# Kernel optimization log

Measured on AMD Instinct MI355X. Metric: run time of the kernel, lower is better.

## Reference

```python
import jax, jax.numpy as jnp
import numpy as np

MODES = 8
WIDTH = 20
LAYERS = 4
TI = 20
B, SX, SY, T = 4, 128, 128, 20


def setup_inputs() -> dict:
    key = jax.random.key(0)
    ks = jax.random.split(key, 12)
    scale = 1.0 / (WIDTH * WIDTH)
    x = jax.random.normal(ks[0], (B, SX, SY, T), jnp.float32)
    # spectral weights: 4 corner blocks per layer, complex stored as real/imag
    spec_wr = scale * jax.random.uniform(ks[1], (LAYERS, 4, WIDTH, WIDTH, MODES, MODES, MODES), jnp.float32)
    spec_wi = scale * jax.random.uniform(ks[2], (LAYERS, 4, WIDTH, WIDTH, MODES, MODES, MODES), jnp.float32)
    conv_w = 0.1 * jax.random.normal(ks[3], (LAYERS, WIDTH, WIDTH), jnp.float32)  # 1x1 conv over channels
    conv_b = 0.01 * jax.random.normal(ks[4], (LAYERS, WIDTH), jnp.float32)
    fc0_w = 0.05 * jax.random.normal(ks[5], (TI + 3, WIDTH), jnp.float32)
    fc0_b = jnp.zeros((WIDTH,), jnp.float32)
    fc1_w = 0.05 * jax.random.normal(ks[6], (WIDTH, 128), jnp.float32)
    fc1_b = jnp.zeros((128,), jnp.float32)
    fc2_w = 0.05 * jax.random.normal(ks[7], (128, 1), jnp.float32)
    fc2_b = jnp.zeros((1,), jnp.float32)
    return {"x": x, "spec_wr": spec_wr, "spec_wi": spec_wi, "conv_w": conv_w,
            "conv_b": conv_b, "fc0_w": fc0_w, "fc0_b": fc0_b, "fc1_w": fc1_w,
            "fc1_b": fc1_b, "fc2_w": fc2_w, "fc2_b": fc2_b}


def _spectral_conv(h, w):
    # h: [B, C, X, Y, Z] real; w: [4, C, C, m, m, m] complex
    b, c, X, Y, Z = h.shape
    m = MODES
    hft = jnp.fft.rfftn(h, axes=(-3, -2, -1))  # [B,C,X,Y,Z//2+1]
    mul = lambda a, wt: jnp.einsum('bixyz,ioxyz->boxyz', a, wt)
    out = jnp.zeros((b, c, X, Y, Z // 2 + 1), jnp.complex64)
    out = out.at[:, :, :m, :m, :m].set(mul(hft[:, :, :m, :m, :m], w[0]))
    out = out.at[:, :, -m:, :m, :m].set(mul(hft[:, :, -m:, :m, :m], w[1]))
    out = out.at[:, :, :m, -m:, :m].set(mul(hft[:, :, :m, -m:, :m], w[2]))
    out = out.at[:, :, -m:, -m:, :m].set(mul(hft[:, :, -m:, -m:, :m], w[3]))
    return jnp.fft.irfftn(out, s=(X, Y, Z), axes=(-3, -2, -1))


def reference(x, spec_wr, spec_wi, conv_w, conv_b, fc0_w, fc0_b, fc1_w, fc1_b, fc2_w, fc2_b):
    b, sx, sy, st = x.shape
    f32 = x.dtype
    # grids in [0,1]; gridt = linspace(0,1,T+1)[1:]
    gx = jnp.linspace(0.0, 1.0, sx, dtype=f32)[None, :, None, None, None]
    gy = jnp.linspace(0.0, 1.0, sy, dtype=f32)[None, None, :, None, None]
    gt = jnp.linspace(0.0, 1.0, st + 1, dtype=f32)[1:][None, None, None, :, None]
    shp = (b, sx, sy, st, 1)
    xr = jnp.broadcast_to(x[:, :, :, None, :], (b, sx, sy, st, st))  # repeat over new T axis
    feat = jnp.concatenate([jnp.broadcast_to(gx, shp), jnp.broadcast_to(gy, shp),
                            jnp.broadcast_to(gt, shp), xr], axis=-1)  # [B,Sx,Sy,T,T+3]
    h = feat @ fc0_w + fc0_b                       # [B,Sx,Sy,T,W]
    h = jnp.transpose(h, (0, 4, 1, 2, 3))          # [B,W,Sx,Sy,T]
    for l in range(LAYERS):
        w = (spec_wr[l] + 1j * spec_wi[l]).astype(jnp.complex64)
        sup = _spectral_conv(h, w)
        inf = jnp.einsum('bixyz,oi->boxyz', h, conv_w[l]) + conv_b[l][None, :, None, None, None]
        h = jax.nn.relu(sup + inf)
    h = jnp.transpose(h, (0, 2, 3, 4, 1))          # [B,Sx,Sy,T,W]
    h = jax.nn.relu(h @ fc1_w + fc1_b)
    out = h @ fc2_w + fc2_b                        # [B,Sx,Sy,T,1]
    return out
```

## Files before the change

kernel.cpp:

```cpp
#include <hip/hip_runtime.h>


#define BB 4
#define CC 20
#define NX 128
#define NY 128
#define NZ 20
#define MM 8
#define NKX 16
#define NKY 16
#define NKZ 8
#define CH_STRIDE (NX * NY * NZ)

#define OFF_H    0u
#define OFF_T1   26214400u
#define OFF_T2   32768000u
#define OFF_A    33587200u
#define OFF_AOUT 33914880u
#define OFF_WXY  34242560u
#define OFF_WZ   34246656u

__global__ void k_tables(float* __restrict__ Wxy, float* __restrict__ Wz) {
    int tid = blockIdx.x * blockDim.x + threadIdx.x;
    const double PI2 = 6.283185307179586476925286766559;
    if (tid < NX * NKX) {
        int y = tid >> 4, ki = tid & 15;
        int kphys = (ki < MM) ? ki : (NX - NKX + ki);
        int p = (y * kphys) & (NX - 1);
        double ang = -PI2 * (double)p / (double)NX;
        Wxy[2 * tid]     = (float)cos(ang);
        Wxy[2 * tid + 1] = (float)sin(ang);
    } else if (tid < NX * NKX + NZ * NKZ) {
        int t = tid - NX * NKX;
        int z = t >> 3, kz = t & 7;
        int p = (z * kz) % NZ;
        double ang = -PI2 * (double)p / (double)NZ;
        Wz[2 * t]     = (float)cos(ang);
        Wz[2 * t + 1] = (float)sin(ang);
    }
}

__global__ __launch_bounds__(256) void k_fc0(const float* __restrict__ x,
                                             const float* __restrict__ w0,
                                             const float* __restrict__ b0,
                                             float* __restrict__ h) {
    int tid = blockIdx.x * blockDim.x + threadIdx.x;
    if (tid >= BB * CC * NX * NY) return;
    int y = tid & 127;
    int r = tid >> 7;
    int xx = r & 127; r >>= 7;
    int c = r % CC;
    int b = r / CC;
    const float* xp = x + (((size_t)(b * NX + xx)) * NY + y) * NZ;
    float base = b0[c] + ((float)xx / 127.0f) * w0[0 * CC + c]
                       + ((float)y  / 127.0f) * w0[1 * CC + c];
#pragma unroll
    for (int k = 0; k < 20; k++) base = fmaf(xp[k], w0[(3 + k) * CC + c], base);
    float wt = w0[2 * CC + c];
    float* hp = h + (size_t)tid * NZ;
#pragma unroll
    for (int t = 0; t < 20; t++) hp[t] = base + ((float)(t + 1) / 20.0f) * wt;
}

__global__ __launch_bounds__(320) void k_dft_y(const float* __restrict__ h,
                                               const float* __restrict__ Wxy,
                                               float* __restrict__ t1) {
    __shared__ __align__(16) float tile[4 * NY * NZ];
    __shared__ __align__(16) float tw[NX * NKX * 2];
    int bid = blockIdx.x;
    int bc = bid >> 5, xg = bid & 31;
    const float* hp = h + ((size_t)bc * NX + xg * 4) * (NY * NZ);
    for (int i = threadIdx.x; i < 4 * NY * NZ; i += 320) tile[i] = hp[i];
    for (int i = threadIdx.x; i < NX * NKX * 2; i += 320) tw[i] = Wxy[i];
    __syncthreads();
    int xl = threadIdx.x / 80;
    int rest = threadIdx.x % 80;
    int ki = rest / 5;
    int z0 = (rest % 5) * 4;
    const float* tp = tile + xl * (NY * NZ);
    float sr0 = 0, sr1 = 0, sr2 = 0, sr3 = 0, si0 = 0, si1 = 0, si2 = 0, si3 = 0;
    for (int y = 0; y < NY; y++) {
        const float4 v = *(const float4*)&tp[y * NZ + z0];
        const float2 w = *(const float2*)&tw[(y * NKX + ki) * 2];
        sr0 = fmaf(v.x, w.x, sr0); si0 = fmaf(v.x, w.y, si0);
        sr1 = fmaf(v.y, w.x, sr1); si1 = fmaf(v.y, w.y, si1);
        sr2 = fmaf(v.z, w.x, sr2); si2 = fmaf(v.z, w.y, si2);
        sr3 = fmaf(v.w, w.x, sr3); si3 = fmaf(v.w, w.y, si3);
    }
    int x = xg * 4 + xl;
    float* o = t1 + (((size_t)bc * NX + x) * NKY + ki) * (NZ * 2) + z0 * 2;
    float4 o0 = {sr0, si0, sr1, si1};
    float4 o1 = {sr2, si2, sr3, si3};
    *(float4*)&o[0] = o0;
    *(float4*)&o[4] = o1;
}

__global__ __launch_bounds__(320) void k_dft_x(const float* __restrict__ t1,
                                               const float* __restrict__ Wxy,
                                               float* __restrict__ t2) {
    __shared__ __align__(16) float tile[NX * NZ * 2];
    __shared__ __align__(16) float tw[NX * NKX * 2];
    int bid = blockIdx.x;
    int bc = bid >> 4, kyi = bid & 15;
    const float* base = t1 + ((size_t)bc * NX * NKY * NZ + (size_t)kyi * NZ) * 2;
    for (int i = threadIdx.x; i < NX * NZ * 2; i += 320) {
        int xx = i / (NZ * 2), r2 = i % (NZ * 2);
        tile[i] = base[(size_t)xx * (NKY * NZ * 2) + r2];
    }
    for (int i = threadIdx.x; i < NX * NKX * 2; i += 320) tw[i] = Wxy[i];
    __syncthreads();
    int ki = threadIdx.x / NZ, z = threadIdx.x % NZ;
    float sr = 0.f, si = 0.f;
    for (int xx = 0; xx < NX; xx++) {
        const float2 a = *(const float2*)&tile[xx * (NZ * 2) + z * 2];
        const float2 w = *(const float2*)&tw[(xx * NKX + ki) * 2];
        sr += a.x * w.x - a.y * w.y;
        si += a.x * w.y + a.y * w.x;
    }
    float* o = t2 + ((((size_t)bc * NKX + ki) * NKY + kyi) * NZ + z) * 2;
    o[0] = sr; o[1] = si;
}

__global__ __launch_bounds__(256) void k_dft_z(const float* __restrict__ t2,
                                               const float* __restrict__ Wz,
                                               float* __restrict__ A) {
    int tid = blockIdx.x * blockDim.x + threadIdx.x;
    if (tid >= BB * CC * NKX * NKY * NKZ) return;
    int kz = tid & 7;
    int rest = tid >> 3;
    const float* p = t2 + (size_t)rest * (NZ * 2);
    float sr = 0.f, si = 0.f;
#pragma unroll
    for (int z = 0; z < NZ; z++) {
        float2 a = *(const float2*)&p[2 * z];
        float2 w = *(const float2*)&Wz[(z * NKZ + kz) * 2];
        sr += a.x * w.x - a.y * w.y;
        si += a.x * w.y + a.y * w.x;
    }
    A[2 * tid] = sr; A[2 * tid + 1] = si;
}

__global__ __launch_bounds__(256) void k_modemix(const float* __restrict__ A,
                                                 const float* __restrict__ wr,
                                                 const float* __restrict__ wi,
                                                 float* __restrict__ Aout, int layer) {
    int tid = blockIdx.x * blockDim.x + threadIdx.x;
    if (tid >= BB * CC * NKX * NKY * NKZ) return;
    int kz = tid & 7;
    int t = tid >> 3;
    int kyi = t & 15; t >>= 4;
    int kxi = t & 15; t >>= 4;
    int o = t % CC;
    int b = t / CC;
    int q = (kxi >= MM ? 1 : 0) + (kyi >= MM ? 2 : 0);
    int mx = kxi & 7, my = kyi & 7;
    size_t wbase = ((size_t)(layer * 4 + q) * (CC * CC) + o) * 512
                 + (size_t)(mx * 64 + my * 8 + kz);
    const float* Ab = A + ((size_t)b * CC * 2048 + (size_t)((kxi * NKY + kyi) * NKZ + kz)) * 2;
    float sr = 0.f, si = 0.f;
#pragma unroll
    for (int i = 0; i < CC; i++) {
        float ar = Ab[(size_t)i * 4096], ai = Ab[(size_t)i * 4096 + 1];
        float wrv = wr[wbase + (size_t)i * (CC * 512)];
        float wiv = wi[wbase + (size_t)i * (CC * 512)];
        sr += ar * wrv - ai * wiv;
        si += ar * wiv + ai * wrv;
    }
    float sc = (kz == 0 ? 1.0f : 2.0f) / 327680.0f;
    Aout[2 * tid] = sr * sc; Aout[2 * tid + 1] = si * sc;
}

__global__ __launch_bounds__(256) void k_invz(const float* __restrict__ Aout,
                                              const float* __restrict__ Wz,
                                              float* __restrict__ u1) {
    int tid = blockIdx.x * blockDim.x + threadIdx.x;
    if (tid >= BB * CC * NKX * NKY * NZ) return;
    int z = tid % NZ;
    int rest = tid / NZ;
    const float* p = Aout + (size_t)rest * (NKZ * 2);
    float sr = 0.f, si = 0.f;
#pragma unroll
    for (int kz = 0; kz < NKZ; kz++) {
        float2 a = *(const float2*)&p[2 * kz];
        float c = Wz[(z * NKZ + kz) * 2], s = -Wz[(z * NKZ + kz) * 2 + 1];
        sr += a.x * c - a.y * s;
        si += a.x * s + a.y * c;
    }
    u1[2 * tid] = sr; u1[2 * tid + 1] = si;
}

__global__ __launch_bounds__(256) void k_invx(const float* __restrict__ u1,
                                              const float* __restrict__ Wxy,
                                              float* __restrict__ u2) {
    int tid = blockIdx.x * blockDim.x + threadIdx.x;
    if (tid >= BB * CC * NX * NKY * NZ) return;
    int z = tid % NZ;
    int t = tid / NZ;
    int kyi = t & 15; t >>= 4;
    int x = t & 127;
    int bo = t >> 7;
    const float* p = u1 + ((size_t)bo * (NKX * NKY * NZ) + (size_t)(kyi * NZ + z)) * 2;
    float sr = 0.f, si = 0.f;
#pragma unroll
    for (int kxi = 0; kxi < NKX; kxi++) {
        float2 a = *(const float2*)&p[(size_t)kxi * (NKY * NZ * 2)];
        float c = Wxy[(x * NKX + kxi) * 2], s = -Wxy[(x * NKX + kxi) * 2 + 1];
        sr += a.x * c - a.y * s;
        si += a.x * s + a.y * c;
    }
    u2[2 * tid] = sr; u2[2 * tid + 1] = si;
}

__global__ __launch_bounds__(256) void k_final(const float* __restrict__ u2,
                                               const float* __restrict__ Wxy,
                                               const float* __restrict__ cw,
                                               const float* __restrict__ cb,
                                               float* __restrict__ h) {
    __shared__ __align__(16) float su2[CC * NKY * NZ * 2];
    int bid = blockIdx.x;
    int half = bid & 1;
    int x = (bid >> 1) & 127;
    int b = bid >> 8;
    for (int i = threadIdx.x; i < CC * NKY * NZ * 2; i += 256) {
        int o = i / (NKY * NZ * 2), r = i % (NKY * NZ * 2);
        su2[i] = u2[((size_t)(b * CC + o) * NX + x) * (NKY * NZ * 2) + r];
    }
    __syncthreads();
    for (int k = 0; k < 5; k++) {
        int sid = threadIdx.x + 256 * k + 1280 * half;
        int y = sid / NZ, z = sid % NZ;
        float cy[NKY], sy[NKY];
#pragma unroll
        for (int kyi = 0; kyi < NKY; kyi++) {
            float2 w = *(const float2*)&Wxy[(y * NKX + kyi) * 2];
            cy[kyi] = w.x; sy[kyi] = w.y;
        }
        size_t hbase = (size_t)b * CC * CH_STRIDE + (size_t)x * (NY * NZ) + (size_t)(y * NZ + z);
        float hv[CC];
#pragma unroll
        for (int i = 0; i < CC; i++) hv[i] = h[hbase + (size_t)i * CH_STRIDE];
        for (int o = 0; o < CC; o++) {
            float acc = cb[o];
#pragma unroll
            for (int i = 0; i < CC; i++) acc = fmaf(cw[o * CC + i], hv[i], acc);
            const float* up = &su2[o * (NKY * NZ * 2) + z * 2];
            float sup = 0.f;
#pragma unroll
            for (int kyi = 0; kyi < NKY; kyi++) {
                float2 u = *(const float2*)&up[kyi * (NZ * 2)];
                sup = fmaf(u.x, cy[kyi], sup);
                sup = fmaf(u.y, sy[kyi], sup);
            }
            float v = acc + sup;
            h[hbase + (size_t)o * CH_STRIDE] = v > 0.f ? v : 0.f;
        }
    }
}

__global__ __launch_bounds__(256) void k_head(const float* __restrict__ h,
                                              const float* __restrict__ w1,
                                              const float* __restrict__ b1,
                                              const float* __restrict__ w2,
                                              const float* __restrict__ b2,
                                              float* __restrict__ out) {
    __shared__ __align__(16) float sw1[CC * 128];
    __shared__ __align__(16) float sb1[128];
    __shared__ __align__(16) float sw2[128];
    for (int i = threadIdx.x; i < CC * 128; i += 256) sw1[i] = w1[i];
    if (threadIdx.x < 128) {
        sb1[threadIdx.x] = b1[threadIdx.x];
        sw2[threadIdx.x] = w2[threadIdx.x];
    }
    __syncthreads();
    int base = blockIdx.x * 1024 + threadIdx.x;
    float hv[4][CC];
    size_t ob[4];
#pragma unroll
    for (int s = 0; s < 4; s++) {
        int tid = base + 256 * s;
        int t = tid % NZ;
        int r = tid / NZ;
        int y = r & 127; r >>= 7;
        int x = r & 127;
        int b = r >> 7;
        size_t hbase = (size_t)b * CC * CH_STRIDE + (size_t)x * (NY * NZ) + (size_t)(y * NZ + t);
        ob[s] = (size_t)tid;
#pragma unroll
        for (int c = 0; c < CC; c++) hv[s][c] = h[hbase + (size_t)c * CH_STRIDE];
    }
    float acc0 = b2[0], acc1 = b2[0], acc2 = b2[0], acc3 = b2[0];
    for (int jc = 0; jc < 32; jc++) {
        const float4 sb = *(const float4*)&sb1[jc * 4];
        float4 s0 = sb, s1 = sb, s2 = sb, s3 = sb;
#pragma unroll
        for (int c = 0; c < CC; c++) {
            const float4 w = *(const float4*)&sw1[c * 128 + jc * 4];
            s0.x = fmaf(hv[0][c], w.x, s0.x); s0.y = fmaf(hv[0][c], w.y, s0.y);
            s0.z = fmaf(hv[0][c], w.z, s0.z); s0.w = fmaf(hv[0][c], w.w, s0.w);
            s1.x = fmaf(hv[1][c], w.x, s1.x); s1.y = fmaf(hv[1][c], w.y, s1.y);
            s1.z = fmaf(hv[1][c], w.z, s1.z); s1.w = fmaf(hv[1][c], w.w, s1.w);
            s2.x = fmaf(hv[2][c], w.x, s2.x); s2.y = fmaf(hv[2][c], w.y, s2.y);
            s2.z = fmaf(hv[2][c], w.z, s2.z); s2.w = fmaf(hv[2][c], w.w, s2.w);
            s3.x = fmaf(hv[3][c], w.x, s3.x); s3.y = fmaf(hv[3][c], w.y, s3.y);
            s3.z = fmaf(hv[3][c], w.z, s3.z); s3.w = fmaf(hv[3][c], w.w, s3.w);
        }
        const float4 v2 = *(const float4*)&sw2[jc * 4];
        acc0 = fmaf(fmaxf(s0.x, 0.f), v2.x, acc0); acc0 = fmaf(fmaxf(s0.y, 0.f), v2.y, acc0);
        acc0 = fmaf(fmaxf(s0.z, 0.f), v2.z, acc0); acc0 = fmaf(fmaxf(s0.w, 0.f), v2.w, acc0);
        acc1 = fmaf(fmaxf(s1.x, 0.f), v2.x, acc1); acc1 = fmaf(fmaxf(s1.y, 0.f), v2.y, acc1);
        acc1 = fmaf(fmaxf(s1.z, 0.f), v2.z, acc1); acc1 = fmaf(fmaxf(s1.w, 0.f), v2.w, acc1);
        acc2 = fmaf(fmaxf(s2.x, 0.f), v2.x, acc2); acc2 = fmaf(fmaxf(s2.y, 0.f), v2.y, acc2);
        acc2 = fmaf(fmaxf(s2.z, 0.f), v2.z, acc2); acc2 = fmaf(fmaxf(s2.w, 0.f), v2.w, acc2);
        acc3 = fmaf(fmaxf(s3.x, 0.f), v2.x, acc3); acc3 = fmaf(fmaxf(s3.y, 0.f), v2.y, acc3);
        acc3 = fmaf(fmaxf(s3.z, 0.f), v2.z, acc3); acc3 = fmaf(fmaxf(s3.w, 0.f), v2.w, acc3);
    }
    out[ob[0]] = acc0;
    out[ob[1]] = acc1;
    out[ob[2]] = acc2;
    out[ob[3]] = acc3;
}

extern "C" void kernel_launch(void* const* d_in, const int* in_sizes, int n_in,
                              void* d_out, int out_size, void* d_ws, size_t ws_size,
                              hipStream_t stream) {
    const float* x       = (const float*)d_in[0];
    const float* spec_wr = (const float*)d_in[1];
    const float* spec_wi = (const float*)d_in[2];
    const float* conv_w  = (const float*)d_in[3];
    const float* conv_b  = (const float*)d_in[4];
    const float* fc0_w   = (const float*)d_in[5];
    const float* fc0_b   = (const float*)d_in[6];
    const float* fc1_w   = (const float*)d_in[7];
    const float* fc1_b   = (const float*)d_in[8];
    const float* fc2_w   = (const float*)d_in[9];
    const float* fc2_b   = (const float*)d_in[10];

    float* ws   = (float*)d_ws;
    float* h    = ws + OFF_H;
    float* t1   = ws + OFF_T1;
    float* t2   = ws + OFF_T2;
    float* A    = ws + OFF_A;
    float* Aout = ws + OFF_AOUT;
    float* Wxy  = ws + OFF_WXY;
    float* Wz   = ws + OFF_WZ;

    hipLaunchKernelGGL(k_tables, dim3(9), dim3(256), 0, stream, Wxy, Wz);
    hipLaunchKernelGGL(k_fc0, dim3(5120), dim3(256), 0, stream, x, fc0_w, fc0_b, h);
    for (int l = 0; l < 4; l++) {
        hipLaunchKernelGGL(k_dft_y, dim3(2560), dim3(320), 0, stream, h, Wxy, t1);
        hipLaunchKernelGGL(k_dft_x, dim3(1280), dim3(320), 0, stream, t1, Wxy, t2);
        hipLaunchKernelGGL(k_dft_z, dim3(640), dim3(256), 0, stream, t2, Wz, A);
        hipLaunchKernelGGL(k_modemix, dim3(640), dim3(256), 0, stream, A, spec_wr, spec_wi, Aout, l);
        hipLaunchKernelGGL(k_invz, dim3(1600), dim3(256), 0, stream, Aout, Wz, t2);
        hipLaunchKernelGGL(k_invx, dim3(12800), dim3(256), 0, stream, t2, Wxy, t1);
        hipLaunchKernelGGL(k_final, dim3(1024), dim3(256), 0, stream, t1, Wxy,
                           conv_w + l * (CC * CC), conv_b + l * CC, h);
    }
    hipLaunchKernelGGL(k_head, dim3(1280), dim3(256), 0, stream,
                       h, fc1_w, fc1_b, fc2_w, fc2_b, (float*)d_out);
}
```

Measured before the change: 1.188 ms.

## Exploit y/y+64 twiddle symmetry in k_final to share inverse-y DFT sums

```diff
diff --git a/kernel.cpp b/kernel.cpp
--- a/kernel.cpp
+++ b/kernel.cpp
@@ -217,42 +217,54 @@
                                                const float* __restrict__ cb,
                                                float* __restrict__ h) {
     __shared__ __align__(16) float su2[CC * NKY * NZ * 2];
-    int bid = blockIdx.x;
-    int half = bid & 1;
-    int x = (bid >> 1) & 127;
-    int b = bid >> 8;
-    for (int i = threadIdx.x; i < CC * NKY * NZ * 2; i += 256) {
-        int o = i / (NKY * NZ * 2), r = i % (NKY * NZ * 2);
-        su2[i] = u2[((size_t)(b * CC + o) * NX + x) * (NKY * NZ * 2) + r];
+    int b = blockIdx.x >> 7, x = blockIdx.x & 127;
+    for (int i4 = threadIdx.x; i4 < (CC * NKY * NZ * 2) / 4; i4 += 256) {
+        int o = i4 / 160, r4 = i4 % 160;
+        *(float4*)&su2[o * 640 + r4 * 4] =
+            *(const float4*)&u2[((size_t)(b * CC + o) * NX + x) * 640 + r4 * 4];
     }
     __syncthreads();
     for (int k = 0; k < 5; k++) {
-        int sid = threadIdx.x + 256 * k + 1280 * half;
-        int y = sid / NZ, z = sid % NZ;
+        int p = threadIdx.x + 256 * k;
+        int z = p % NZ;
+        int y = p / NZ;
         float cy[NKY], sy[NKY];
 #pragma unroll
         for (int kyi = 0; kyi < NKY; kyi++) {
             float2 w = *(const float2*)&Wxy[(y * NKX + kyi) * 2];
             cy[kyi] = w.x; sy[kyi] = w.y;
         }
-        size_t hbase = (size_t)b * CC * CH_STRIDE + (size_t)x * (NY * NZ) + (size_t)(y * NZ + z);
-        float hv[CC];
-#pragma unroll
-        for (int i = 0; i < CC; i++) hv[i] = h[hbase + (size_t)i * CH_STRIDE];
+        size_t hbase_a = (size_t)b * CC * CH_STRIDE + (size_t)x * (NY * NZ) + (size_t)(y * NZ + z);
+        size_t hbase_b = hbase_a + (size_t)(64 * NZ);
+        float hva[CC], hvb[CC];
+#pragma unroll
+        for (int i = 0; i < CC; i++) {
+            hva[i] = h[hbase_a + (size_t)i * CH_STRIDE];
+            hvb[i] = h[hbase_b + (size_t)i * CH_STRIDE];
+        }
         for (int o = 0; o < CC; o++) {
-            float acc = cb[o];
-#pragma unroll
-            for (int i = 0; i < CC; i++) acc = fmaf(cw[o * CC + i], hv[i], acc);
+            float acca = cb[o], accb = cb[o];
+#pragma unroll
+            for (int i = 0; i < CC; i++) {
+                float w = cw[o * CC + i];
+                acca = fmaf(w, hva[i], acca);
+                accb = fmaf(w, hvb[i], accb);
+            }
             const float* up = &su2[o * (NKY * NZ * 2) + z * 2];
-            float sup = 0.f;
-#pragma unroll
-            for (int kyi = 0; kyi < NKY; kyi++) {
-                float2 u = *(const float2*)&up[kyi * (NZ * 2)];
-                sup = fmaf(u.x, cy[kyi], sup);
-                sup = fmaf(u.y, sy[kyi], sup);
+            float se = 0.f, so = 0.f;
+#pragma unroll
+            for (int kk = 0; kk < 8; kk++) {
+                float2 ue = *(const float2*)&up[(2 * kk) * (NZ * 2)];
+                se = fmaf(ue.x, cy[2 * kk], se);
+                se = fmaf(ue.y, sy[2 * kk], se);
+                float2 uo = *(const float2*)&up[(2 * kk + 1) * (NZ * 2)];
+                so = fmaf(uo.x, cy[2 * kk + 1], so);
+                so = fmaf(uo.y, sy[2 * kk + 1], so);
             }
-            float v = acc + sup;
-            h[hbase + (size_t)o * CH_STRIDE] = v > 0.f ? v : 0.f;
+            float va = acca + (se + so);
+            float vb = accb + (se - so);
+            h[hbase_a + (size_t)o * CH_STRIDE] = va > 0.f ? va : 0.f;
+            h[hbase_b + (size_t)o * CH_STRIDE] = vb > 0.f ? vb : 0.f;
         }
     }
 }
@@ -353,7 +365,7 @@
         hipLaunchKernelGGL(k_modemix, dim3(640), dim3(256), 0, stream, A, spec_wr, spec_wi, Aout, l);
         hipLaunchKernelGGL(k_invz, dim3(1600), dim3(256), 0, stream, Aout, Wz, t2);
         hipLaunchKernelGGL(k_invx, dim3(12800), dim3(256), 0, stream, t2, Wxy, t1);
-        hipLaunchKernelGGL(k_final, dim3(1024), dim3(256), 0, stream, t1, Wxy,
+        hipLaunchKernelGGL(k_final, dim3(512), dim3(256), 0, stream, t1, Wxy,
                            conv_w + l * (CC * CC), conv_b + l * CC, h);
     }
     hipLaunchKernelGGL(k_head, dim3(1280), dim3(256), 0, stream,
```

Measured after the change: 1.012 ms. 14.8% less time.
